# Optimization experiments

Measured on AMD Instinct MI355X. Metric: run time of the kernel, lower is better.

## Reference

```python
import jax, jax.numpy as jnp
import numpy as np

N = 50000   # nodes
E = 800000  # edges
F_IN, F_HID, F_OUT = 128, 96, 40


def setup_inputs() -> dict:
    key = jax.random.key(0)
    ks = jax.random.split(key, 9)
    x = jax.random.normal(ks[0], (N, F_IN), dtype=jnp.float32)
    edge_index = jax.random.randint(ks[1], (2, E), 0, N, dtype=jnp.int32)
    def lin(k, fi, fo):
        s = 1.0 / np.sqrt(fi)
        return jax.random.uniform(k, (fi, fo), jnp.float32, -s, s)
    W1 = lin(ks[2], F_IN, F_HID)
    b1 = jnp.zeros((F_HID,), jnp.float32)
    W2 = lin(ks[3], F_HID, F_HID)
    b2 = jnp.zeros((F_HID,), jnp.float32)
    Wout = lin(ks[4], F_HID, F_OUT)
    bout = jnp.zeros((F_OUT,), jnp.float32)
    return {"x": x, "edge_index": edge_index, "W1": W1, "b1": b1,
            "W2": W2, "b2": b2, "Wout": Wout, "bout": bout}


def _gcn_norm(edge_index, n):
    # add self-loops, symmetric degree normalization (PyG GCNConv default)
    loops = jnp.arange(n, dtype=edge_index.dtype)
    src = jnp.concatenate([edge_index[0], loops])
    dst = jnp.concatenate([edge_index[1], loops])
    deg = jax.ops.segment_sum(jnp.ones_like(dst, dtype=jnp.float32), dst,
                              num_segments=n)
    dinv = jnp.where(deg > 0, jax.lax.rsqrt(deg), 0.0)
    norm = dinv[src] * dinv[dst]   # [E+N]
    return src, dst, norm


def _gcn_layer(h, src, dst, norm, W, b, n):
    # linear transform, then normalized scatter-add aggregation, then bias
    h = h @ W                                 # [N, Fout]
    msg = h[src] * norm[:, None]              # gather + scale
    agg = jax.ops.segment_sum(msg, dst, num_segments=n)
    return agg + b


def reference(x, edge_index, W1, b1, W2, b2, Wout, bout):
    n = x.shape[0]
    src, dst, norm = _gcn_norm(edge_index, n)
    h = jax.nn.relu(_gcn_layer(x, src, dst, norm, W1, b1, n))
    h = jax.nn.relu(_gcn_layer(h, src, dst, norm, W2, b2, n))
    return h @ Wout + bout
```

## Files before the change

kernel.cpp:

```cpp
#include <hip/hip_runtime.h>
#include <hip/hip_fp16.h>

#define N_NODES 50000
#define N_EDGES 800000
#define F_INN   128
#define F_HID   96
#define F_OUTT  40

typedef _Float16 half8 __attribute__((ext_vector_type(8)));
typedef float    floatx4 __attribute__((ext_vector_type(4)));

template <int FI, typename TIN>
__device__ __forceinline__ void mfma_gemm_body(
        const TIN* __restrict__ X, const __half* __restrict__ BTg,
        float4* __restrict__ Th4, int n, int bx) {
    __shared__ __half BTl[96 * 136];
    __shared__ __half OUTl[4 * 16 * 104];
    int tid = threadIdx.x;
    {
        const int4* s = reinterpret_cast<const int4*>(BTg);
        int4* d = reinterpret_cast<int4*>(BTl);
        for (int i = tid; i < 96 * 136 / 8; i += 256) d[i] = s[i];
    }
    __syncthreads();

    int lane = tid & 63, w = tid >> 6;
    int lm = lane & 15, q = lane >> 4;
    int base = bx * 64 + w * 16;
    int node = base + lm;
    int nclamp = min(node, n - 1);
    const TIN* Xrow = X + (size_t)nclamp * FI;

    floatx4 cf[6];
    #pragma unroll
    for (int t = 0; t < 6; ++t) cf[t] = (floatx4){0.f, 0.f, 0.f, 0.f};

    constexpr int KS = FI / 32;
    #pragma unroll
    for (int ks = 0; ks < KS; ++ks) {
        half8 bv;
        if constexpr (sizeof(TIN) == 4) {
            const float4* xr = reinterpret_cast<const float4*>(Xrow + 32 * ks + q * 8);
            float4 f0 = xr[0], f1 = xr[1];
            union { half8 v; __half2 h[4]; } b;
            b.h[0] = __floats2half2_rn(f0.x, f0.y);
            b.h[1] = __floats2half2_rn(f0.z, f0.w);
            b.h[2] = __floats2half2_rn(f1.x, f1.y);
            b.h[3] = __floats2half2_rn(f1.z, f1.w);
            bv = b.v;
        } else {
            bv = *reinterpret_cast<const half8*>(Xrow + 32 * ks + q * 8);
        }
        #pragma unroll
        for (int t = 0; t < 6; ++t) {
            half8 a = *reinterpret_cast<const half8*>(
                &BTl[(t * 16 + lm) * 136 + q * 8 + 32 * ks]);
            cf[t] = __builtin_amdgcn_mfma_f32_16x16x32_f16(a, bv, cf[t], 0, 0, 0);
        }
    }

    __half* orow = OUTl + (w * 16 + lm) * 104;
    #pragma unroll
    for (int t = 0; t < 6; ++t) {
        union { int2 i2; __half2 h[2]; } u;
        u.h[0] = __floats2half2_rn(cf[t][0], cf[t][1]);
        u.h[1] = __floats2half2_rn(cf[t][2], cf[t][3]);
        *reinterpret_cast<int2*>(&orow[t * 16 + q * 4]) = u.i2;
    }
    #pragma unroll
    for (int R = 0; R < 3; ++R) {
        int nl = lane >> 2, c = (lane & 3) + 4 * R;
        float4 v = *reinterpret_cast<const float4*>(&OUTl[(w * 16 + nl) * 104 + c * 8]);
        int gn = base + nl;
        if (gn < n) Th4[(size_t)gn * 12 + c] = v;
    }
}

__global__ __launch_bounds__(256) void count_gemm1_kernel(
        const int* __restrict__ dst, int* __restrict__ counts4, int* __restrict__ rank,
        int e, const float* __restrict__ X, const __half* __restrict__ BT1,
        float4* __restrict__ Th4, int n, int nCB) {
    if ((int)blockIdx.x < nCB) {
        int i = blockIdx.x * 256 + threadIdx.x;
        if (i < e) rank[i] = atomicAdd(&counts4[dst[i] * 4 + (i & 3)], 1);
    } else {
        mfma_gemm_body<F_INN, float>(X, BT1, Th4, n, blockIdx.x - nCB);
    }
}

template <int FI, typename TIN>
__global__ __launch_bounds__(256) void mfma_gemm_kernel(
        const TIN* __restrict__ X, const __half* __restrict__ BTg,
        float4* __restrict__ Th4, int n) {
    mfma_gemm_body<FI, TIN>(X, BTg, Th4, n, blockIdx.x);
}

__global__ void wt_kernel(const float* __restrict__ W1, const float* __restrict__ W2,
                          __half* __restrict__ BT1, __half* __restrict__ BT2) {
    int i = blockIdx.x * 256 + threadIdx.x;
    if (i < 96 * 128) {
        int j = i / 128, k = i - j * 128;
        BT1[j * 136 + k] = __float2half(W1[k * 96 + j]);
    } else if (i < 96 * 128 + 96 * 96) {
        int t = i - 96 * 128;
        int j = t / 96, k = t - j * 96;
        BT2[j * 136 + k] = __float2half(W2[k * 96 + j]);
    }
}

__global__ __launch_bounds__(1024) void scan_local_kernel(
        const int4* __restrict__ counts4, int* __restrict__ row_start,
        float* __restrict__ dinv, int* __restrict__ blk_sums, int n) {
    __shared__ int wave_sums[16];
    int tid = threadIdx.x, lane = tid & 63, wid = tid >> 6;
    int i = blockIdx.x * 1024 + tid;
    int v = 0;
    if (i < n) {
        int4 c = counts4[i];
        v = c.x + c.y + c.z + c.w;
    }
    int val = v;
    #pragma unroll
    for (int off = 1; off < 64; off <<= 1) {
        int u = __shfl_up(val, off, 64);
        if (lane >= off) val += u;
    }
    if (lane == 63) wave_sums[wid] = val;
    __syncthreads();
    if (wid == 0) {
        int w = (lane < 16) ? wave_sums[lane] : 0;
        #pragma unroll
        for (int off = 1; off < 16; off <<= 1) {
            int u = __shfl_up(w, off, 64);
            if (lane >= off) w += u;
        }
        if (lane < 16) wave_sums[lane] = w;
    }
    __syncthreads();
    int excl = ((wid == 0) ? 0 : wave_sums[wid - 1]) + (val - v);
    if (i < n) {
        row_start[i] = excl;
        dinv[i] = rsqrtf((float)(v + 1));
    }
    if (tid == 0) blk_sums[blockIdx.x] = wave_sums[15];
}

__global__ __launch_bounds__(1024) void scan_apply_kernel(
        int* __restrict__ row_start, const int* __restrict__ blk_sums,
        const int4* __restrict__ counts4, int4* __restrict__ base4, int n, int nblk) {
    __shared__ int s_my, s_tot;
    int tid = threadIdx.x;
    if (tid < 64) {
        int v = (tid < nblk) ? blk_sums[tid] : 0;
        int val = v;
        #pragma unroll
        for (int off = 1; off < 64; off <<= 1) {
            int u = __shfl_up(val, off, 64);
            if (tid >= off) val += u;
        }
        if (tid == (int)blockIdx.x) s_my = val - v;
        if (tid == 63) s_tot = val;
    }
    __syncthreads();
    int i = blockIdx.x * 1024 + tid;
    if (i < n) {
        int4 c = counts4[i];
        int b = row_start[i] + s_my;
        row_start[i] = b;
        base4[i] = make_int4(b, b + c.x, b + c.x + c.y, b + c.x + c.y + c.z);
    }
    if (blockIdx.x == 0 && tid == 0) row_start[n] = s_tot;
}

__global__ void fill_csr_kernel(const int* __restrict__ src, const int* __restrict__ dst,
                                const int* __restrict__ rank, const int* __restrict__ base4,
                                int* __restrict__ csr_src, int e) {
    int i = blockIdx.x * blockDim.x + threadIdx.x;
    if (i >= e) return;
    csr_src[base4[dst[i] * 4 + (i & 3)] + rank[i]] = src[i];
}

__global__ __launch_bounds__(256) void agg_kernel(
        const __half2* __restrict__ T, const int* __restrict__ row_start,
        const int* __restrict__ csr_src, const float* __restrict__ dinv,
        const float* __restrict__ bias, __half2* __restrict__ H, int n) {
    int lane = threadIdx.x & 63;
    int node = __builtin_amdgcn_readfirstlane(blockIdx.x * 4 + (threadIdx.x >> 6));
    if (node >= n) return;
    int fl = min(lane, 47);

    float dn = dinv[node];
    float2 self = __half22float2(T[(size_t)node * 48 + fl]);
    float accx = dn * self.x, accy = dn * self.y;

    int idx = row_start[node];
    int end = row_start[node + 1];
    for (; idx + 8 <= end; idx += 8) {
        int s[8];
        #pragma unroll
        for (int u = 0; u < 8; ++u) s[u] = csr_src[idx + u];
        float ws[8];
        #pragma unroll
        for (int u = 0; u < 8; ++u) ws[u] = dinv[s[u]];
        float2 f[8];
        #pragma unroll
        for (int u = 0; u < 8; ++u) f[u] = __half22float2(T[(size_t)s[u] * 48 + fl]);
        #pragma unroll
        for (int u = 0; u < 8; ++u) {
            accx = fmaf(ws[u], f[u].x, accx);
            accy = fmaf(ws[u], f[u].y, accy);
        }
    }
    for (; idx < end; ++idx) {
        int s = csr_src[idx];
        float w = dinv[s];
        float2 f = __half22float2(T[(size_t)s * 48 + fl]);
        accx = fmaf(w, f.x, accx);
        accy = fmaf(w, f.y, accy);
    }
    if (lane < 48) {
        float2 b = reinterpret_cast<const float2*>(bias)[lane];
        float ox = fmaxf(fmaf(dn, accx, b.x), 0.f);
        float oy = fmaxf(fmaf(dn, accy, b.y), 0.f);
        H[(size_t)node * 48 + lane] = __floats2half2_rn(ox, oy);
    }
}

__global__ __launch_bounds__(320) void gemm_out_kernel(
        const __half2* __restrict__ A, const float* __restrict__ W,
        const float* __restrict__ bias, float* __restrict__ C, int n) {
    __shared__ float Wlds[96 * 40];
    int tid = threadIdx.y * 10 + threadIdx.x;
    for (int i = tid; i < 96 * 10; i += 320)
        reinterpret_cast<float4*>(Wlds)[i] = reinterpret_cast<const float4*>(W)[i];
    __syncthreads();

    int j    = threadIdx.x * 4;
    int node = blockIdx.x * 32 + threadIdx.y;
    int nc   = min(node, n - 1);
    const __half2* Ah = A + (size_t)nc * 48;
    float4 acc = make_float4(0.f, 0.f, 0.f, 0.f);
    for (int k2 = 0; k2 < 48; k2 += 2) {
        float2 a01 = __half22float2(Ah[k2]);
        float2 a23 = __half22float2(Ah[k2 + 1]);
        int k = 2 * k2;
        float4 w0 = *reinterpret_cast<const float4*>(Wlds + (k + 0) * 40 + j);
        float4 w1 = *reinterpret_cast<const float4*>(Wlds + (k + 1) * 40 + j);
        float4 w2 = *reinterpret_cast<const float4*>(Wlds + (k + 2) * 40 + j);
        float4 w3 = *reinterpret_cast<const float4*>(Wlds + (k + 3) * 40 + j);
        acc.x += a01.x * w0.x + a01.y * w1.x + a23.x * w2.x + a23.y * w3.x;
        acc.y += a01.x * w0.y + a01.y * w1.y + a23.x * w2.y + a23.y * w3.y;
        acc.z += a01.x * w0.z + a01.y * w1.z + a23.x * w2.z + a23.y * w3.z;
        acc.w += a01.x * w0.w + a01.y * w1.w + a23.x * w2.w + a23.y * w3.w;
    }
    if (node < n) {
        float4 b = *reinterpret_cast<const float4*>(bias + j);
        acc.x += b.x; acc.y += b.y; acc.z += b.z; acc.w += b.w;
        *reinterpret_cast<float4*>(C + (size_t)node * 40 + j) = acc;
    }
}


extern "C" void kernel_launch(void* const* d_in, const int* in_sizes, int n_in,
                              void* d_out, int out_size, void* d_ws, size_t ws_size,
                              hipStream_t stream) {
    const float* x    = (const float*)d_in[0];
    const int*   ei   = (const int*)d_in[1];
    const float* W1   = (const float*)d_in[2];
    const float* b1   = (const float*)d_in[3];
    const float* W2   = (const float*)d_in[4];
    const float* b2   = (const float*)d_in[5];
    const float* Wout = (const float*)d_in[6];
    const float* bout = (const float*)d_in[7];
    float*       out  = (float*)d_out;

    const int* src = ei;
    const int* dst = ei + N_EDGES;

    char* ws = (char*)d_ws;
    size_t off = 0;
    auto alloc = [&](size_t bytes) {
        size_t o = off;
        off = (off + bytes + 511) & ~(size_t)511;
        return (void*)(ws + o);
    };
    int*     counts4   = (int*)    alloc((size_t)N_NODES * 4 * sizeof(int));
    int4*    base4     = (int4*)   alloc((size_t)N_NODES * sizeof(int4));
    int*     row_start = (int*)    alloc((N_NODES + 1) * sizeof(int));
    float*   dinv      = (float*)  alloc(N_NODES * sizeof(float));
    int*     blk_sums  = (int*)    alloc(64 * sizeof(int));
    int*     rank      = (int*)    alloc((size_t)N_EDGES * sizeof(int));
    int*     csr_src   = (int*)    alloc((size_t)N_EDGES * sizeof(int));
    __half*  BT1       = (__half*) alloc((size_t)96 * 136 * sizeof(__half));
    __half*  BT2       = (__half*) alloc((size_t)96 * 136 * sizeof(__half));
    __half2* Th        = (__half2*)alloc((size_t)N_NODES * 48 * sizeof(__half2));
    __half2* Hh        = (__half2*)alloc((size_t)N_NODES * 48 * sizeof(__half2));

    const int NSCAN = (N_NODES + 1023) / 1024;
    const int CB    = (N_EDGES + 255) / 256;
    const int GB    = (N_NODES + 63) / 64;

    hipMemsetAsync(counts4, 0, (size_t)N_NODES * 4 * sizeof(int), stream);
    wt_kernel<<<(96 * 128 + 96 * 96 + 255) / 256, 256, 0, stream>>>(W1, W2, BT1, BT2);

    count_gemm1_kernel<<<CB + GB, 256, 0, stream>>>(
        dst, counts4, rank, N_EDGES, x, BT1, (float4*)Th, N_NODES, CB);

    scan_local_kernel<<<NSCAN, 1024, 0, stream>>>(
        (const int4*)counts4, row_start, dinv, blk_sums, N_NODES);
    scan_apply_kernel<<<NSCAN, 1024, 0, stream>>>(
        row_start, blk_sums, (const int4*)counts4, base4, N_NODES, NSCAN);
    fill_csr_kernel<<<CB, 256, 0, stream>>>(
        src, dst, rank, (const int*)base4, csr_src, N_EDGES);

    agg_kernel<<<(N_NODES + 3) / 4, 256, 0, stream>>>(
        Th, row_start, csr_src, dinv, b1, Hh, N_NODES);

    mfma_gemm_kernel<F_HID, __half><<<GB, 256, 0, stream>>>(
        (const __half*)Hh, BT2, (float4*)Th, N_NODES);
    agg_kernel<<<(N_NODES + 3) / 4, 256, 0, stream>>>(
        Th, row_start, csr_src, dinv, b2, Hh, N_NODES);

    gemm_out_kernel<<<(N_NODES + 31) / 32, dim3(10, 32), 0, stream>>>(
        Hh, Wout, bout, out, N_NODES);
}
```

Measured before the change: 227.7 us.

## Vectorize edge gather across lanes and fuse output GEMM into second aggregation

Rewrites the aggregation kernel so each wavefront processes five edges at once, with 12 lanes each loading 16-byte half8 chunks of a neighbor's features, then reduces across edge groups with shuffles. The self-loop is folded into the same loop. A templated variant stages Wout in LDS and computes the final 96x40 projection per node, removing the separate output GEMM kernel and the round-trip of the second hidden layer through global memory. The cost is extra LDS, a block barrier, and partially idle lanes during the tail GEMM.

```diff
diff --git a/kernel.cpp b/kernel.cpp
--- a/kernel.cpp
+++ b/kernel.cpp
@@ -180,83 +180,103 @@
     csr_src[base4[dst[i] * 4 + (i & 3)] + rank[i]] = src[i];
 }
 
+template <bool FUSE_OUT>
 __global__ __launch_bounds__(256) void agg_kernel(
         const __half2* __restrict__ T, const int* __restrict__ row_start,
         const int* __restrict__ csr_src, const float* __restrict__ dinv,
-        const float* __restrict__ bias, __half2* __restrict__ H, int n) {
-    int lane = threadIdx.x & 63;
-    int node = __builtin_amdgcn_readfirstlane(blockIdx.x * 4 + (threadIdx.x >> 6));
-    if (node >= n) return;
-    int fl = min(lane, 47);
-
-    float dn = dinv[node];
-    float2 self = __half22float2(T[(size_t)node * 48 + fl]);
-    float accx = dn * self.x, accy = dn * self.y;
-
-    int idx = row_start[node];
-    int end = row_start[node + 1];
-    for (; idx + 8 <= end; idx += 8) {
-        int s[8];
+        const float* __restrict__ bias, __half2* __restrict__ H,
+        const float* __restrict__ Wout, const float* __restrict__ bout,
+        float* __restrict__ out, int n) {
+    __shared__ float Wl[96 * 40];
+    __shared__ float Hs[4][96];
+    int tid = threadIdx.x;
+    if (FUSE_OUT) {
+        const float4* ws = reinterpret_cast<const float4*>(Wout);
+        float4* wd = reinterpret_cast<float4*>(Wl);
+        for (int i = tid; i < 960; i += 256) wd[i] = ws[i];
+    }
+
+    int lane = tid & 63, wid = tid >> 6;
+    int node = __builtin_amdgcn_readfirstlane(blockIdx.x * 4 + wid);
+    int nodec = min(node, n - 1);
+    int e = lane / 12;
+    int g = lane - e * 12;
+
+    float dn = dinv[nodec];
+    int idx = row_start[nodec], end = row_start[nodec + 1];
+    const __half* Tb = reinterpret_cast<const __half*>(T);
+
+    float acc[8];
+    #pragma unroll
+    for (int j = 0; j < 8; ++j) acc[j] = 0.f;
+
+    auto ITER = [&](int base) {
+        int p = base + e;
+        int s = nodec; float w = 0.f;
+        if (e < 5) {
+            if (p >= idx && p < end) { s = csr_src[p]; w = dinv[s]; }
+            else if (p == idx - 1)   { w = dn; }
+        }
+        union { half8 v; __half2 h[4]; } u;
+        u.v = *reinterpret_cast<const half8*>(Tb + (size_t)s * 96 + g * 8);
         #pragma unroll
-        for (int u = 0; u < 8; ++u) s[u] = csr_src[idx + u];
-        float ws[8];
-        #pragma unroll
-        for (int u = 0; u < 8; ++u) ws[u] = dinv[s[u]];
-        float2 f[8];
-        #pragma unroll
-        for (int u = 0; u < 8; ++u) f[u] = __half22float2(T[(size_t)s[u] * 48 + fl]);
-        #pragma unroll
-        for (int u = 0; u < 8; ++u) {
-            accx = fmaf(ws[u], f[u].x, accx);
-            accy = fmaf(ws[u], f[u].y, accy);
-        }
-    }
-    for (; idx < end; ++idx) {
-        int s = csr_src[idx];
-        float w = dinv[s];
-        float2 f = __half22float2(T[(size_t)s * 48 + fl]);
-        accx = fmaf(w, f.x, accx);
-        accy = fmaf(w, f.y, accy);
-    }
-    if (lane < 48) {
-        float2 b = reinterpret_cast<const float2*>(bias)[lane];
-        float ox = fmaxf(fmaf(dn, accx, b.x), 0.f);
-        float oy = fmaxf(fmaf(dn, accy, b.y), 0.f);
-        H[(size_t)node * 48 + lane] = __floats2half2_rn(ox, oy);
-    }
-}
-
-__global__ __launch_bounds__(320) void gemm_out_kernel(
-        const __half2* __restrict__ A, const float* __restrict__ W,
-        const float* __restrict__ bias, float* __restrict__ C, int n) {
-    __shared__ float Wlds[96 * 40];
-    int tid = threadIdx.y * 10 + threadIdx.x;
-    for (int i = tid; i < 96 * 10; i += 320)
-        reinterpret_cast<float4*>(Wlds)[i] = reinterpret_cast<const float4*>(W)[i];
-    __syncthreads();
-
-    int j    = threadIdx.x * 4;
-    int node = blockIdx.x * 32 + threadIdx.y;
-    int nc   = min(node, n - 1);
-    const __half2* Ah = A + (size_t)nc * 48;
-    float4 acc = make_float4(0.f, 0.f, 0.f, 0.f);
-    for (int k2 = 0; k2 < 48; k2 += 2) {
-        float2 a01 = __half22float2(Ah[k2]);
-        float2 a23 = __half22float2(Ah[k2 + 1]);
-        int k = 2 * k2;
-        float4 w0 = *reinterpret_cast<const float4*>(Wlds + (k + 0) * 40 + j);
-        float4 w1 = *reinterpret_cast<const float4*>(Wlds + (k + 1) * 40 + j);
-        float4 w2 = *reinterpret_cast<const float4*>(Wlds + (k + 2) * 40 + j);
-        float4 w3 = *reinterpret_cast<const float4*>(Wlds + (k + 3) * 40 + j);
-        acc.x += a01.x * w0.x + a01.y * w1.x + a23.x * w2.x + a23.y * w3.x;
-        acc.y += a01.x * w0.y + a01.y * w1.y + a23.x * w2.y + a23.y * w3.y;
-        acc.z += a01.x * w0.z + a01.y * w1.z + a23.x * w2.z + a23.y * w3.z;
-        acc.w += a01.x * w0.w + a01.y * w1.w + a23.x * w2.w + a23.y * w3.w;
-    }
-    if (node < n) {
-        float4 b = *reinterpret_cast<const float4*>(bias + j);
-        acc.x += b.x; acc.y += b.y; acc.z += b.z; acc.w += b.w;
-        *reinterpret_cast<float4*>(C + (size_t)node * 40 + j) = acc;
+        for (int q = 0; q < 4; ++q) {
+            float2 f = __half22float2(u.h[q]);
+            acc[2 * q]     = fmaf(w, f.x, acc[2 * q]);
+            acc[2 * q + 1] = fmaf(w, f.y, acc[2 * q + 1]);
+        }
+    };
+    for (int base = idx - 1; base < end; base += 10) { ITER(base); ITER(base + 5); }
+
+    float red[8];
+    #pragma unroll
+    for (int j = 0; j < 8; ++j) {
+        float t = acc[j];
+        t += __shfl(acc[j], lane + 12);
+        t += __shfl(acc[j], lane + 24);
+        t += __shfl(acc[j], lane + 36);
+        t += __shfl(acc[j], lane + 48);
+        red[j] = t;
+    }
+
+    if (lane < 12 && node < n) {
+        const float4* bp = reinterpret_cast<const float4*>(bias);
+        float4 b0 = bp[2 * lane], b1 = bp[2 * lane + 1];
+        float r[8];
+        r[0] = fmaxf(fmaf(dn, red[0], b0.x), 0.f);
+        r[1] = fmaxf(fmaf(dn, red[1], b0.y), 0.f);
+        r[2] = fmaxf(fmaf(dn, red[2], b0.z), 0.f);
+        r[3] = fmaxf(fmaf(dn, red[3], b0.w), 0.f);
+        r[4] = fmaxf(fmaf(dn, red[4], b1.x), 0.f);
+        r[5] = fmaxf(fmaf(dn, red[5], b1.y), 0.f);
+        r[6] = fmaxf(fmaf(dn, red[6], b1.z), 0.f);
+        r[7] = fmaxf(fmaf(dn, red[7], b1.w), 0.f);
+        if (!FUSE_OUT) {
+            union { int4 i4; __half2 h[4]; } o;
+            o.h[0] = __floats2half2_rn(r[0], r[1]);
+            o.h[1] = __floats2half2_rn(r[2], r[3]);
+            o.h[2] = __floats2half2_rn(r[4], r[5]);
+            o.h[3] = __floats2half2_rn(r[6], r[7]);
+            *reinterpret_cast<int4*>(H + (size_t)node * 48 + lane * 4) = o.i4;
+        } else {
+            #pragma unroll
+            for (int j = 0; j < 8; ++j) Hs[wid][lane * 8 + j] = r[j];
+        }
+    }
+
+    if (FUSE_OUT) {
+        __syncthreads();
+        if (tid < 160) {
+            int nn = tid / 40, j = tid - nn * 40;
+            int gn = blockIdx.x * 4 + nn;
+            if (gn < n) {
+                float a = bout[j];
+                const float* hrow = Hs[nn];
+                #pragma unroll 8
+                for (int k = 0; k < 96; ++k) a = fmaf(hrow[k], Wl[k * 40 + j], a);
+                out[(size_t)gn * 40 + j] = a;
+            }
+        }
     }
 }
 
@@ -299,6 +319,7 @@
     const int NSCAN = (N_NODES + 1023) / 1024;
     const int CB    = (N_EDGES + 255) / 256;
     const int GB    = (N_NODES + 63) / 64;
+    const int AB    = (N_NODES + 3) / 4;
 
     hipMemsetAsync(counts4, 0, (size_t)N_NODES * 4 * sizeof(int), stream);
     wt_kernel<<<(96 * 128 + 96 * 96 + 255) / 256, 256, 0, stream>>>(W1, W2, BT1, BT2);
@@ -313,14 +334,11 @@
     fill_csr_kernel<<<CB, 256, 0, stream>>>(
         src, dst, rank, (const int*)base4, csr_src, N_EDGES);
 
-    agg_kernel<<<(N_NODES + 3) / 4, 256, 0, stream>>>(
-        Th, row_start, csr_src, dinv, b1, Hh, N_NODES);
+    agg_kernel<false><<<AB, 256, 0, stream>>>(
+        Th, row_start, csr_src, dinv, b1, Hh, Wout, bout, out, N_NODES);
 
     mfma_gemm_kernel<F_HID, __half><<<GB, 256, 0, stream>>>(
         (const __half*)Hh, BT2, (float4*)Th, N_NODES);
-    agg_kernel<<<(N_NODES + 3) / 4, 256, 0, stream>>>(
-        Th, row_start, csr_src, dinv, b2, Hh, N_NODES);
-
-    gemm_out_kernel<<<(N_NODES + 31) / 32, dim3(10, 32), 0, stream>>>(
-        Hh, Wout, bout, out, N_NODES);
-}
+    agg_kernel<true><<<AB, 256, 0, stream>>>(
+        Th, row_start, csr_src, dinv, b2, Hh, Wout, bout, out, N_NODES);
+}
```

Result: slower. 245.2 us (+7.7%).

## Slice hidden features into four 24-wide planes and restructure aggregation per slice

Applied to the files above, without the earlier changes.

Stores the 96-wide fp16 hidden tensors as four separate 24-column slices so each aggregation block gathers only one slice. Block IDs are interleaved so that blocks working on different slices of the same node group run close together, which keeps each slice's working set smaller and more cache-resident. The aggregation kernel is rewritten so 16 lanes per node cover five edges times three 16-byte chunks, with the self-loop folded into the edge loop and a DPP cross-lane reduction at the end. The GEMM producer and consumer kernels are adapted to the new layout. In exchange the gathers per edge are smaller and the code adds reduction overhead and lane underutilisation (15 of 16 lanes active).

```diff
diff --git a/kernel.cpp b/kernel.cpp
--- a/kernel.cpp
+++ b/kernel.cpp
@@ -6,6 +6,10 @@
 #define F_INN   128
 #define F_HID   96
 #define F_OUTT  40
+
+#define SL_HALVES (N_NODES * 24)
+#define SL_F4     (N_NODES * 3)
+#define NGRP      3125
 
 typedef _Float16 half8 __attribute__((ext_vector_type(8)));
 typedef float    floatx4 __attribute__((ext_vector_type(4)));
@@ -29,7 +33,6 @@
     int base = bx * 64 + w * 16;
     int node = base + lm;
     int nclamp = min(node, n - 1);
-    const TIN* Xrow = X + (size_t)nclamp * FI;
 
     floatx4 cf[6];
     #pragma unroll
@@ -40,7 +43,8 @@
     for (int ks = 0; ks < KS; ++ks) {
         half8 bv;
         if constexpr (sizeof(TIN) == 4) {
-            const float4* xr = reinterpret_cast<const float4*>(Xrow + 32 * ks + q * 8);
+            const float4* xr = reinterpret_cast<const float4*>(
+                X + (size_t)nclamp * FI + 32 * ks + q * 8);
             float4 f0 = xr[0], f1 = xr[1];
             union { half8 v; __half2 h[4]; } b;
             b.h[0] = __floats2half2_rn(f0.x, f0.y);
@@ -49,7 +53,11 @@
             b.h[3] = __floats2half2_rn(f1.z, f1.w);
             bv = b.v;
         } else {
-            bv = *reinterpret_cast<const half8*>(Xrow + 32 * ks + q * 8);
+            int c8 = 4 * ks + q;
+            int sl = c8 / 3, of8 = c8 - sl * 3;
+            bv = *reinterpret_cast<const half8*>(
+                reinterpret_cast<const _Float16*>(X) +
+                (size_t)sl * SL_HALVES + (size_t)nclamp * 24 + of8 * 8);
         }
         #pragma unroll
         for (int t = 0; t < 6; ++t) {
@@ -70,9 +78,10 @@
     #pragma unroll
     for (int R = 0; R < 3; ++R) {
         int nl = lane >> 2, c = (lane & 3) + 4 * R;
+        int sl = c / 3, of8 = c - sl * 3;
         float4 v = *reinterpret_cast<const float4*>(&OUTl[(w * 16 + nl) * 104 + c * 8]);
         int gn = base + nl;
-        if (gn < n) Th4[(size_t)gn * 12 + c] = v;
+        if (gn < n) Th4[(size_t)sl * SL_F4 + (size_t)gn * 3 + of8] = v;
     }
 }
 
@@ -180,54 +189,82 @@
     csr_src[base4[dst[i] * 4 + (i & 3)] + rank[i]] = src[i];
 }
 
+template <int N>
+__device__ __forceinline__ float dpp_shl(float x) {
+    return __int_as_float(__builtin_amdgcn_update_dpp(
+        0, __float_as_int(x), 0x100 + N, 0xF, 0xF, true));
+}
+
 __global__ __launch_bounds__(256) void agg_kernel(
-        const __half2* __restrict__ T, const int* __restrict__ row_start,
+        const __half* __restrict__ T, const int* __restrict__ row_start,
         const int* __restrict__ csr_src, const float* __restrict__ dinv,
-        const float* __restrict__ bias, __half2* __restrict__ H, int n) {
-    int lane = threadIdx.x & 63;
-    int node = __builtin_amdgcn_readfirstlane(blockIdx.x * 4 + (threadIdx.x >> 6));
-    if (node >= n) return;
-    int fl = min(lane, 47);
-
+        const float* __restrict__ bias, __half* __restrict__ H, int n) {
+    int bid = blockIdx.x;
+    int xr = bid & 7, m = bid >> 3;
+    int s  = xr >> 1;
+    int grp = m * 2 + (xr & 1);
+    if (grp >= NGRP) return;
+
+    int tid = threadIdx.x, lane = tid & 63, wid = tid >> 6;
+    int e5 = lane & 15;
+    int e  = e5 / 3;
+    int g  = e5 - e * 3;
+    bool act = e5 < 15;
+
+    int node = grp * 16 + wid * 4 + (lane >> 4);
     float dn = dinv[node];
-    float2 self = __half22float2(T[(size_t)node * 48 + fl]);
-    float accx = dn * self.x, accy = dn * self.y;
-
-    int idx = row_start[node];
-    int end = row_start[node + 1];
-    for (; idx + 8 <= end; idx += 8) {
-        int s[8];
-        #pragma unroll
-        for (int u = 0; u < 8; ++u) s[u] = csr_src[idx + u];
-        float ws[8];
-        #pragma unroll
-        for (int u = 0; u < 8; ++u) ws[u] = dinv[s[u]];
-        float2 f[8];
-        #pragma unroll
-        for (int u = 0; u < 8; ++u) f[u] = __half22float2(T[(size_t)s[u] * 48 + fl]);
-        #pragma unroll
-        for (int u = 0; u < 8; ++u) {
-            accx = fmaf(ws[u], f[u].x, accx);
-            accy = fmaf(ws[u], f[u].y, accy);
-        }
-    }
-    for (; idx < end; ++idx) {
-        int s = csr_src[idx];
-        float w = dinv[s];
-        float2 f = __half22float2(T[(size_t)s * 48 + fl]);
-        accx = fmaf(w, f.x, accx);
-        accy = fmaf(w, f.y, accy);
-    }
-    if (lane < 48) {
-        float2 b = reinterpret_cast<const float2*>(bias)[lane];
-        float ox = fmaxf(fmaf(dn, accx, b.x), 0.f);
-        float oy = fmaxf(fmaf(dn, accy, b.y), 0.f);
-        H[(size_t)node * 48 + lane] = __floats2half2_rn(ox, oy);
+    int idx = row_start[node], end = row_start[node + 1];
+    const _Float16* Ts = reinterpret_cast<const _Float16*>(T) + (size_t)s * SL_HALVES;
+
+    float acc[8];
+    #pragma unroll
+    for (int t = 0; t < 8; ++t) acc[t] = 0.f;
+
+    auto ROUND = [&](int q) {
+        int sn = node; float w = 0.f;
+        if (act && q < end) {
+            if (q >= idx) { sn = csr_src[q]; w = dinv[sn]; }
+            else          { w = dn; }
+        }
+        union { half8 v; __half2 h[4]; } u;
+        u.v = *reinterpret_cast<const half8*>(Ts + (size_t)sn * 24 + g * 8);
+        #pragma unroll
+        for (int t = 0; t < 4; ++t) {
+            float2 f = __half22float2(u.h[t]);
+            acc[2 * t]     = fmaf(w, f.x, acc[2 * t]);
+            acc[2 * t + 1] = fmaf(w, f.y, acc[2 * t + 1]);
+        }
+    };
+    int p = idx - 1 + e;
+    do { ROUND(p); ROUND(p + 5); p += 10; } while (__any(act && p < end));
+
+    float tot[8];
+    #pragma unroll
+    for (int t = 0; t < 8; ++t) {
+        float v1 = acc[t] + dpp_shl<3>(acc[t]);
+        float v2 = v1 + dpp_shl<6>(v1);
+        tot[t] = v2 + dpp_shl<12>(acc[t]);
+    }
+
+    if (e5 < 3) {
+        const float4* bp = reinterpret_cast<const float4*>(bias + s * 24 + e5 * 8);
+        float4 b0 = bp[0], b1 = bp[1];
+        union { int4 i4; __half2 h[4]; } o;
+        o.h[0] = __floats2half2_rn(fmaxf(fmaf(dn, tot[0], b0.x), 0.f),
+                                   fmaxf(fmaf(dn, tot[1], b0.y), 0.f));
+        o.h[1] = __floats2half2_rn(fmaxf(fmaf(dn, tot[2], b0.z), 0.f),
+                                   fmaxf(fmaf(dn, tot[3], b0.w), 0.f));
+        o.h[2] = __floats2half2_rn(fmaxf(fmaf(dn, tot[4], b1.x), 0.f),
+                                   fmaxf(fmaf(dn, tot[5], b1.y), 0.f));
+        o.h[3] = __floats2half2_rn(fmaxf(fmaf(dn, tot[6], b1.z), 0.f),
+                                   fmaxf(fmaf(dn, tot[7], b1.w), 0.f));
+        *reinterpret_cast<int4*>(
+            H + (size_t)s * SL_HALVES + (size_t)node * 24 + e5 * 8) = o.i4;
     }
 }
 
 __global__ __launch_bounds__(320) void gemm_out_kernel(
-        const __half2* __restrict__ A, const float* __restrict__ W,
+        const __half* __restrict__ A, const float* __restrict__ W,
         const float* __restrict__ bias, float* __restrict__ C, int n) {
     __shared__ float Wlds[96 * 40];
     int tid = threadIdx.y * 10 + threadIdx.x;
@@ -238,20 +275,24 @@
     int j    = threadIdx.x * 4;
     int node = blockIdx.x * 32 + threadIdx.y;
     int nc   = min(node, n - 1);
-    const __half2* Ah = A + (size_t)nc * 48;
     float4 acc = make_float4(0.f, 0.f, 0.f, 0.f);
-    for (int k2 = 0; k2 < 48; k2 += 2) {
-        float2 a01 = __half22float2(Ah[k2]);
-        float2 a23 = __half22float2(Ah[k2 + 1]);
-        int k = 2 * k2;
-        float4 w0 = *reinterpret_cast<const float4*>(Wlds + (k + 0) * 40 + j);
-        float4 w1 = *reinterpret_cast<const float4*>(Wlds + (k + 1) * 40 + j);
-        float4 w2 = *reinterpret_cast<const float4*>(Wlds + (k + 2) * 40 + j);
-        float4 w3 = *reinterpret_cast<const float4*>(Wlds + (k + 3) * 40 + j);
-        acc.x += a01.x * w0.x + a01.y * w1.x + a23.x * w2.x + a23.y * w3.x;
-        acc.y += a01.x * w0.y + a01.y * w1.y + a23.x * w2.y + a23.y * w3.y;
-        acc.z += a01.x * w0.z + a01.y * w1.z + a23.x * w2.z + a23.y * w3.z;
-        acc.w += a01.x * w0.w + a01.y * w1.w + a23.x * w2.w + a23.y * w3.w;
+    #pragma unroll
+    for (int c8 = 0; c8 < 12; ++c8) {
+        int sl = c8 / 3, of8 = c8 - sl * 3;
+        union { int4 i4; __half2 h[4]; } u;
+        u.i4 = *reinterpret_cast<const int4*>(
+            A + (size_t)sl * SL_HALVES + (size_t)nc * 24 + of8 * 8);
+        #pragma unroll
+        for (int t = 0; t < 4; ++t) {
+            float2 a = __half22float2(u.h[t]);
+            int k = c8 * 8 + 2 * t;
+            float4 w0 = *reinterpret_cast<const float4*>(Wlds + k * 40 + j);
+            float4 w1 = *reinterpret_cast<const float4*>(Wlds + (k + 1) * 40 + j);
+            acc.x += a.x * w0.x + a.y * w1.x;
+            acc.y += a.x * w0.y + a.y * w1.y;
+            acc.z += a.x * w0.z + a.y * w1.z;
+            acc.w += a.x * w0.w + a.y * w1.w;
+        }
     }
     if (node < n) {
         float4 b = *reinterpret_cast<const float4*>(bias + j);
@@ -293,12 +334,13 @@
     int*     csr_src   = (int*)    alloc((size_t)N_EDGES * sizeof(int));
     __half*  BT1       = (__half*) alloc((size_t)96 * 136 * sizeof(__half));
     __half*  BT2       = (__half*) alloc((size_t)96 * 136 * sizeof(__half));
-    __half2* Th        = (__half2*)alloc((size_t)N_NODES * 48 * sizeof(__half2));
-    __half2* Hh        = (__half2*)alloc((size_t)N_NODES * 48 * sizeof(__half2));
+    __half*  Th        = (__half*) alloc((size_t)N_NODES * 96 * sizeof(__half));
+    __half*  Hh        = (__half*) alloc((size_t)N_NODES * 96 * sizeof(__half));
 
     const int NSCAN = (N_NODES + 1023) / 1024;
     const int CB    = (N_EDGES + 255) / 256;
     const int GB    = (N_NODES + 63) / 64;
+    const int AGB   = ((NGRP + 1) / 2) * 8;
 
     hipMemsetAsync(counts4, 0, (size_t)N_NODES * 4 * sizeof(int), stream);
     wt_kernel<<<(96 * 128 + 96 * 96 + 255) / 256, 256, 0, stream>>>(W1, W2, BT1, BT2);
@@ -313,12 +355,12 @@
     fill_csr_kernel<<<CB, 256, 0, stream>>>(
         src, dst, rank, (const int*)base4, csr_src, N_EDGES);
 
-    agg_kernel<<<(N_NODES + 3) / 4, 256, 0, stream>>>(
+    agg_kernel<<<AGB, 256, 0, stream>>>(
         Th, row_start, csr_src, dinv, b1, Hh, N_NODES);
 
     mfma_gemm_kernel<F_HID, __half><<<GB, 256, 0, stream>>>(
-        (const __half*)Hh, BT2, (float4*)Th, N_NODES);
-    agg_kernel<<<(N_NODES + 3) / 4, 256, 0, stream>>>(
+        Hh, BT2, (float4*)Th, N_NODES);
+    agg_kernel<<<AGB, 256, 0, stream>>>(
         Th, row_start, csr_src, dinv, b2, Hh, N_NODES);
 
     gemm_out_kernel<<<(N_NODES + 31) / 32, dim3(10, 32), 0, stream>>>(
```

Result: slower. 250.8 us (+10.2%).
